# Optimization experiments

Measured on AMD Instinct MI355X. Metric: run time of the kernel, lower is better.

Reference implementation:

```python
import jax, jax.numpy as jnp
import numpy as np

EXP_BITS = 5
SIG_BITS = 10


def fp_quantize_ste(x, exp_bits=EXP_BITS, sig_bits=SIG_BITS):
    """Simulate a low-precision float format (round-to-nearest, subnormals on),
    with a straight-through estimator for gradients."""
    ebias = 2 ** (exp_bits - 1) - 1
    emin = 1 - ebias                      # min normal exponent; below -> subnormal
    emax = ebias
    xmax = (2.0 - 2.0 ** (-sig_bits)) * (2.0 ** emax)

    ax = jnp.abs(x)
    # exponent of each value; guard log2(0)
    e = jnp.floor(jnp.log2(jnp.where(ax > 0, ax, 1.0)))
    # clamping e below emin quantizes subnormals on the fixed 2^(emin-sig_bits) grid;
    # clamping above emax is handled by the final saturation to +-xmax
    e = jnp.clip(e, emin, emax)
    scale = jnp.exp2(sig_bits - e)        # quantization step = 2^(e - sig_bits)
    q = jnp.round(x * scale) / scale      # round-to-nearest (rmode=1)
    q = jnp.clip(q, -xmax, xmax)
    q = jnp.where(ax > 0, q, x)           # preserve exact zeros (and signed zero)
    # straight-through estimator: forward = q, backward = identity
    return x + jax.lax.stop_gradient(q - x)


def setup_inputs() -> dict:
    key = jax.random.key(0)
    k1, k2, k3 = jax.random.split(key, 3)
    N, D_IN, D_OUT = 8192, 4096, 4096
    x = jax.random.normal(k1, (N, D_IN), dtype=jnp.float32)
    weight = jax.random.normal(k2, (D_OUT, D_IN), dtype=jnp.float32) * (D_IN ** -0.5)
    bias = jax.random.normal(k3, (D_OUT,), dtype=jnp.float32) * 0.01
    return {"x": x, "weight": weight, "bias": bias}


def reference(x, weight, bias):
    xq = fp_quantize_ste(x)               # act_quant
    wq = fp_quantize_ste(weight)          # weight_quant
    bq = fp_quantize_ste(bias)            # bias quantized with weight_quant
    # F.linear: x @ W^T + b
    return jnp.einsum('ni,oi->no', xq, wq) + bq
```

## Files before the change

kernel.cpp:

```cpp
#include <hip/hip_runtime.h>
#include <hip/hip_fp16.h>
#include <cstdint>
#include <cstddef>

#define GLOBAL_AS __attribute__((address_space(1)))
#define LDS_AS    __attribute__((address_space(3)))

typedef __attribute__((ext_vector_type(8))) _Float16 f16x8;
typedef __attribute__((ext_vector_type(4))) float    f32x4;

__device__ __forceinline__ void gload_lds16(const void* g, void* l) {
    __builtin_amdgcn_global_load_lds((const GLOBAL_AS void*)g,
                                     (LDS_AS void*)l, 16, 0, 0);
}

__device__ __forceinline__ __half qcvt(float x) {
    x = fminf(fmaxf(x, -65504.f), 65504.f);
    return __float2half(x);
}

__global__ void quant_xw_f32_to_f16(const float* __restrict__ xin, int x4,
                                    const float* __restrict__ win, int w4,
                                    __half* __restrict__ xout,
                                    __half* __restrict__ wout) {
    const int stride = gridDim.x * blockDim.x;
    const int tot = x4 + w4;
    for (int i = blockIdx.x * blockDim.x + threadIdx.x; i < tot; i += stride) {
        const bool isx = (i < x4);
        const int  j   = isx ? i : i - x4;
        const float4 f = reinterpret_cast<const float4*>(isx ? xin : win)[j];
        union { __half h[4]; uint2 u; } p;
        p.h[0] = qcvt(f.x);
        p.h[1] = qcvt(f.y);
        p.h[2] = qcvt(f.z);
        p.h[3] = qcvt(f.w);
        reinterpret_cast<uint2*>(isx ? xout : wout)[j] = p.u;
    }
}

__global__ __launch_bounds__(512, 2) void gemm_f16_8phase(
    const __half* __restrict__ A, const __half* __restrict__ B,
    const float* __restrict__ bias, float* __restrict__ C,
    int M, int N, int K)
{
    __shared__ __align__(16) __half lds[2][2][2][8192];

    const int tid  = threadIdx.x;
    const int lane = tid & 63;
    const int wid  = tid >> 6;
    const int wr   = wid >> 2;
    const int wc   = wid & 3;
    const int fr   = lane & 15;
    const int fq   = lane >> 4;

    const int nwg = gridDim.x;
    const int qq = nwg >> 3, rr = nwg & 7;
    const int xcd = blockIdx.x & 7, idx = blockIdx.x >> 3;
    const int wgid = (xcd < rr ? xcd * (qq + 1)
                               : rr * (qq + 1) + (xcd - rr) * qq) + idx;
    const int nbn = N >> 8;
    const int tile_m = (wgid / nbn) << 8;
    const int tile_n = (wgid % nbn) << 8;

    const int wbyte = (lane * 16) ^ (((lane >> 5) & 1) << 5);
    const int srow  = ((wid >> 1) << 4) + (wbyte >> 6);
    const int scb   = ((wid & 1) << 6) + (wbyte & 63);
    const char* gA0 = (const char*)A + (size_t)(tile_m + srow) * K * 2 + scb;
    const char* gB0 = (const char*)B + (size_t)(tile_n + srow) * K * 2 + scb;
    const size_t rstep = (size_t)64  * K * 2;
    const size_t hstep = (size_t)128 * K * 2;
    const int ldst = tid * 16;

    const int woff = (fr * 64 + fq * 16) ^ (((fr >> 3) & 1) << 5);
    const uint32_t lds0 = (uint32_t)(size_t)(LDS_AS const char*)&lds[0][0][0][0];
    const uint32_t aBase = lds0 + (uint32_t)(wr * 8192 + woff);
    const uint32_t bBase = lds0 + 32768u + (uint32_t)(wc * 4096 + woff);

    f32x4 acc[2][2][4][2];
#pragma unroll
    for (int qa = 0; qa < 2; ++qa)
#pragma unroll
        for (int qb = 0; qb < 2; ++qb)
#pragma unroll
            for (int m = 0; m < 4; ++m)
#pragma unroll
                for (int n = 0; n < 2; ++n)
                    acc[qa][qb][m][n] = (f32x4){0.f, 0.f, 0.f, 0.f};

    f16x8 af[4][2];
    f16x8 bf0[2][2];
    f16x8 bf1[2][2];

#define STAGE_A(bufi, h, kt) do {                                          \
        char* l_ = (char*)(&lds[bufi][0][h][0]) + ldst;                    \
        const char* g_ = gA0 + (size_t)(kt) * 128 + ((h) ? hstep : 0);     \
        gload_lds16(g_, l_);                                               \
        gload_lds16(g_ + rstep, l_ + 8192);                                \
    } while (0)

#define STAGE_B(bufi, h, kt) do {                                          \
        char* l_ = (char*)(&lds[bufi][1][h][0]) + ldst;                    \
        const char* g_ = gB0 + (size_t)(kt) * 128 + ((h) ? hstep : 0);     \
        gload_lds16(g_, l_);                                               \
        gload_lds16(g_ + rstep, l_ + 8192);                                \
    } while (0)

#define DSR(dst, addr, OFF)                                                \
    asm volatile("ds_read_b128 %0, %1 offset:" OFF                         \
                 : "=v"(dst) : "v"(addr))

#define LDGA(bufi, qa) do {                                                \
        const uint32_t a_ = aBase + (bufi) * 65536u + (qa) * 16384u;       \
        DSR(af[0][0], a_, "0");    DSR(af[0][1], a_, "1024");              \
        DSR(af[1][0], a_, "2048"); DSR(af[1][1], a_, "3072");              \
        DSR(af[2][0], a_, "4096"); DSR(af[2][1], a_, "5120");              \
        DSR(af[3][0], a_, "6144"); DSR(af[3][1], a_, "7168");              \
    } while (0)

#define LDGB(dst, bufi, hb) do {                                           \
        const uint32_t b_ = bBase + (bufi) * 65536u + (hb) * 16384u;       \
        DSR(dst[0][0], b_, "0");    DSR(dst[0][1], b_, "1024");            \
        DSR(dst[1][0], b_, "2048"); DSR(dst[1][1], b_, "3072");            \
    } while (0)

#define MMA(qa, qb, BF)                                                    \
    __builtin_amdgcn_s_setprio(1);                                         \
    _Pragma("unroll")                                                      \
    for (int m_ = 0; m_ < 4; ++m_) {                                       \
        _Pragma("unroll")                                                  \
        for (int n_ = 0; n_ < 2; ++n_) {                                   \
            acc[qa][qb][m_][n_] = __builtin_amdgcn_mfma_f32_16x16x32_f16(  \
                af[m_][0], BF[n_][0], acc[qa][qb][m_][n_], 0, 0, 0);       \
            acc[qa][qb][m_][n_] = __builtin_amdgcn_mfma_f32_16x16x32_f16(  \
                af[m_][1], BF[n_][1], acc[qa][qb][m_][n_], 0, 0, 0);       \
        }                                                                  \
    }                                                                      \
    __builtin_amdgcn_s_setprio(0);

#define PH_WAIT_MMA()                                                      \
    __builtin_amdgcn_s_barrier();                                          \
    asm volatile("s_waitcnt lgkmcnt(0)");                                  \
    __builtin_amdgcn_sched_barrier(0)

#define PH_END()                                                           \
    __builtin_amdgcn_s_barrier()

#define TILE_FULL(cur, nxt, kt)                                            \
    LDGB(bf0, cur, 0); LDGA(cur, 0); STAGE_B(nxt, 0, (kt) + 1);            \
    asm volatile("s_waitcnt lgkmcnt(8)");                                  \
    PH_WAIT_MMA(); MMA(0, 0, bf0); PH_END();                               \
    LDGB(bf1, cur, 1); STAGE_A(cur, 0, (kt) + 2);                          \
    PH_WAIT_MMA(); MMA(0, 1, bf1); PH_END();                               \
    LDGA(cur, 1); STAGE_B(cur, 1, (kt) + 2);                               \
    PH_WAIT_MMA(); MMA(1, 1, bf1); PH_END();                               \
    STAGE_A(cur, 1, (kt) + 2);                                             \
    asm volatile("s_waitcnt vmcnt(6)");                                    \
    PH_WAIT_MMA(); MMA(1, 0, bf0); PH_END();

    STAGE_A(0, 0, 0); STAGE_B(0, 0, 0); STAGE_B(0, 1, 0); STAGE_A(0, 1, 0);
    STAGE_A(1, 0, 1); STAGE_B(1, 1, 1); STAGE_A(1, 1, 1);
    asm volatile("s_waitcnt vmcnt(6)");
    __builtin_amdgcn_s_barrier();

    const int nt = K >> 6;
    for (int kt = 0; kt + 3 < nt; kt += 2) {
        TILE_FULL(0, 1, kt);
        TILE_FULL(1, 0, kt + 1);
    }

    LDGB(bf0, 0, 0); LDGA(0, 0); STAGE_B(1, 0, nt - 1);
    PH_WAIT_MMA(); MMA(0, 0, bf0); PH_END();
    LDGB(bf1, 0, 1);
    PH_WAIT_MMA(); MMA(0, 1, bf1); PH_END();
    LDGA(0, 1);
    PH_WAIT_MMA(); MMA(1, 1, bf1); PH_END();
    asm volatile("s_waitcnt vmcnt(0)");
    PH_WAIT_MMA(); MMA(1, 0, bf0); PH_END();

    LDGB(bf0, 1, 0); LDGA(1, 0);
    PH_WAIT_MMA(); MMA(0, 0, bf0); PH_END();
    LDGB(bf1, 1, 1);
    PH_WAIT_MMA(); MMA(0, 1, bf1); PH_END();
    LDGA(1, 1);
    PH_WAIT_MMA(); MMA(1, 1, bf1); PH_END();
    asm volatile("s_waitcnt lgkmcnt(0)");
    __builtin_amdgcn_sched_barrier(0);
    MMA(1, 0, bf0);

    float bv[2][2];
#pragma unroll
    for (int qb = 0; qb < 2; ++qb)
#pragma unroll
        for (int n = 0; n < 2; ++n)
            bv[qb][n] = __half2float(qcvt(
                bias[tile_n + qb * 128 + wc * 32 + n * 16 + fr]));

#pragma unroll
    for (int qa = 0; qa < 2; ++qa)
#pragma unroll
        for (int qb = 0; qb < 2; ++qb)
#pragma unroll
            for (int m = 0; m < 4; ++m)
#pragma unroll
                for (int n = 0; n < 2; ++n) {
                    const int col = tile_n + qb * 128 + wc * 32 + n * 16 + fr;
                    const int rowb = tile_m + qa * 128 + wr * 64 + m * 16 + fq * 4;
#pragma unroll
                    for (int r = 0; r < 4; ++r)
                        C[(size_t)(rowb + r) * N + col] =
                            acc[qa][qb][m][n][r] + bv[qb][n];
                }

#undef STAGE_A
#undef STAGE_B
#undef DSR
#undef LDGA
#undef LDGB
#undef MMA
#undef PH_WAIT_MMA
#undef PH_END
#undef TILE_FULL
}

__global__ void qat_gemm_naive(const float* __restrict__ A,
                               const float* __restrict__ B,
                               const float* __restrict__ bias,
                               float* __restrict__ C, int M, int N, int K) {
    const int col = blockIdx.x * blockDim.x + threadIdx.x;
    const int row = blockIdx.y;
    if (col >= N || row >= M) return;
    float s = 0.f;
    for (int k = 0; k < K; ++k) {
        float a = __half2float(qcvt(A[(size_t)row * K + k]));
        float b = __half2float(qcvt(B[(size_t)col * K + k]));
        s += a * b;
    }
    C[(size_t)row * N + col] = s + __half2float(qcvt(bias[col]));
}

extern "C" void kernel_launch(void* const* d_in, const int* in_sizes, int n_in,
                              void* d_out, int out_size, void* d_ws,
                              size_t ws_size, hipStream_t stream) {
    const float* x = (const float*)d_in[0];
    const float* w = (const float*)d_in[1];
    const float* b = (const float*)d_in[2];
    float* out = (float*)d_out;

    const int xn = in_sizes[0];
    const int wn = in_sizes[1];
    const int N  = in_sizes[2];
    const int K  = wn / N;
    const int M  = xn / K;

    const size_t need = (size_t)(xn + wn) * sizeof(__half);
    const bool ok = (M % 256 == 0) && (N % 256 == 0) &&
                    (K % 128 == 0) && (K >= 256);

    if (ws_size >= need && ok) {
        __half* xq = (__half*)d_ws;
        __half* wq = xq + xn;

        const int x4 = xn / 4, w4 = wn / 4;
        int blk = ((x4 + w4) + 255) / 256; if (blk > 2048) blk = 2048;
        quant_xw_f32_to_f16<<<blk, 256, 0, stream>>>(x, x4, w, w4, xq, wq);

        dim3 grid((M / 256) * (N / 256));
        gemm_f16_8phase<<<grid, 512, 0, stream>>>(xq, wq, b, out, M, N, K);
    } else {
        dim3 grid((N + 255) / 256, M);
        qat_gemm_naive<<<grid, 256, 0, stream>>>(x, w, b, out, M, N, K);
    }
}
```

Baseline: 288.2 us.

## Split MFMA phases on partial LDS waits and prefetch next tile's B fragments

Each MFMA phase is split into two halves gated by partial lgkmcnt waits, so the first half of the MFMAs can start while the remaining ds_reads are still in flight. The B fragments for the next k-tile are loaded during the last phase of the current tile using ping-pong register sets (bfP/bfQ), which removes the LDS read latency at the start of each tile. The per-phase wait-then-barrier sequence is also reorganized. In exchange, register pressure rises from holding the extra B fragments, and correctness now depends on the hand-counted lgkmcnt values matching the issue order.

```diff
diff --git a/kernel.cpp b/kernel.cpp
--- a/kernel.cpp
+++ b/kernel.cpp
@@ -88,8 +88,8 @@
                     acc[qa][qb][m][n] = (f32x4){0.f, 0.f, 0.f, 0.f};
 
     f16x8 af[4][2];
-    f16x8 bf0[2][2];
-    f16x8 bf1[2][2];
+    f16x8 bfP[2][2];
+    f16x8 bfQ[2][2];
 
 #define STAGE_A(bufi, h, kt) do {                                          \
         char* l_ = (char*)(&lds[bufi][0][h][0]) + ldst;                    \
@@ -123,69 +123,116 @@
         DSR(dst[1][0], b_, "2048"); DSR(dst[1][1], b_, "3072");            \
     } while (0)
 
-#define MMA(qa, qb, BF)                                                    \
+#define MMA_PAIR(qa, qb, mm, nn, BF)                                       \
+    acc[qa][qb][mm][nn] = __builtin_amdgcn_mfma_f32_16x16x32_f16(          \
+        af[mm][0], BF[nn][0], acc[qa][qb][mm][nn], 0, 0, 0);               \
+    acc[qa][qb][mm][nn] = __builtin_amdgcn_mfma_f32_16x16x32_f16(          \
+        af[mm][1], BF[nn][1], acc[qa][qb][mm][nn], 0, 0, 0);
+
+#define MMA_M01(qa, qb, BF)                                                \
     __builtin_amdgcn_s_setprio(1);                                         \
-    _Pragma("unroll")                                                      \
-    for (int m_ = 0; m_ < 4; ++m_) {                                       \
-        _Pragma("unroll")                                                  \
-        for (int n_ = 0; n_ < 2; ++n_) {                                   \
-            acc[qa][qb][m_][n_] = __builtin_amdgcn_mfma_f32_16x16x32_f16(  \
-                af[m_][0], BF[n_][0], acc[qa][qb][m_][n_], 0, 0, 0);       \
-            acc[qa][qb][m_][n_] = __builtin_amdgcn_mfma_f32_16x16x32_f16(  \
-                af[m_][1], BF[n_][1], acc[qa][qb][m_][n_], 0, 0, 0);       \
-        }                                                                  \
-    }                                                                      \
+    MMA_PAIR(qa, qb, 0, 0, BF) MMA_PAIR(qa, qb, 0, 1, BF)                  \
+    MMA_PAIR(qa, qb, 1, 0, BF) MMA_PAIR(qa, qb, 1, 1, BF)                  \
     __builtin_amdgcn_s_setprio(0);
 
-#define PH_WAIT_MMA()                                                      \
+#define MMA_M23(qa, qb, BF)                                                \
+    __builtin_amdgcn_s_setprio(1);                                         \
+    MMA_PAIR(qa, qb, 2, 0, BF) MMA_PAIR(qa, qb, 2, 1, BF)                  \
+    MMA_PAIR(qa, qb, 3, 0, BF) MMA_PAIR(qa, qb, 3, 1, BF)                  \
+    __builtin_amdgcn_s_setprio(0);
+
+#define MMA_N0(qa, qb, BF)                                                 \
+    __builtin_amdgcn_s_setprio(1);                                         \
+    MMA_PAIR(qa, qb, 0, 0, BF) MMA_PAIR(qa, qb, 1, 0, BF)                  \
+    MMA_PAIR(qa, qb, 2, 0, BF) MMA_PAIR(qa, qb, 3, 0, BF)                  \
+    __builtin_amdgcn_s_setprio(0);
+
+#define MMA_N1(qa, qb, BF)                                                 \
+    __builtin_amdgcn_s_setprio(1);                                         \
+    MMA_PAIR(qa, qb, 0, 1, BF) MMA_PAIR(qa, qb, 1, 1, BF)                  \
+    MMA_PAIR(qa, qb, 2, 1, BF) MMA_PAIR(qa, qb, 3, 1, BF)                  \
+    __builtin_amdgcn_s_setprio(0);
+
+#define MMA_FULL(qa, qb, BF)                                               \
+    MMA_M01(qa, qb, BF) MMA_M23(qa, qb, BF)
+
+#define WAITL(NLIT)                                                        \
+    asm volatile("s_waitcnt lgkmcnt(" NLIT ")");                           \
+    __builtin_amdgcn_sched_barrier(0)
+
+#define BARS()                                                             \
     __builtin_amdgcn_s_barrier();                                          \
-    asm volatile("s_waitcnt lgkmcnt(0)");                                  \
     __builtin_amdgcn_sched_barrier(0)
 
-#define PH_END()                                                           \
-    __builtin_amdgcn_s_barrier()
-
-#define TILE_FULL(cur, nxt, kt)                                            \
-    LDGB(bf0, cur, 0); LDGA(cur, 0); STAGE_B(nxt, 0, (kt) + 1);            \
-    asm volatile("s_waitcnt lgkmcnt(8)");                                  \
-    PH_WAIT_MMA(); MMA(0, 0, bf0); PH_END();                               \
-    LDGB(bf1, cur, 1); STAGE_A(cur, 0, (kt) + 2);                          \
-    PH_WAIT_MMA(); MMA(0, 1, bf1); PH_END();                               \
+#define TILE_FULL(cur, nxt, kt, B0S, B1S)                                  \
+                \
+    LDGA(cur, 0); STAGE_B(nxt, 0, (kt) + 1);                               \
+    WAITL("4"); MMA_M01(0, 0, B0S);                                        \
+    WAITL("0"); MMA_M23(0, 0, B0S);                                        \
+    BARS();                                                                \
+                    \
+    LDGB(B1S, cur, 1); STAGE_A(cur, 0, (kt) + 2);                          \
+    WAITL("2"); MMA_N0(0, 1, B1S);                                         \
+    WAITL("0"); MMA_N1(0, 1, B1S);                                         \
+    BARS();                                                                \
+                \
     LDGA(cur, 1); STAGE_B(cur, 1, (kt) + 2);                               \
-    PH_WAIT_MMA(); MMA(1, 1, bf1); PH_END();                               \
+    WAITL("4"); MMA_M01(1, 1, B1S);                                        \
+    WAITL("0"); MMA_M23(1, 1, B1S);                                        \
+    BARS();                                                                \
+    \
     STAGE_A(cur, 1, (kt) + 2);                                             \
     asm volatile("s_waitcnt vmcnt(6)");                                    \
-    PH_WAIT_MMA(); MMA(1, 0, bf0); PH_END();
+    BARS();                                                                \
+    LDGB(B1S, nxt, 0);                                                     \
+    __builtin_amdgcn_sched_barrier(0);                                     \
+    MMA_FULL(1, 0, B0S);                                                   \
+    BARS();
 
     STAGE_A(0, 0, 0); STAGE_B(0, 0, 0); STAGE_B(0, 1, 0); STAGE_A(0, 1, 0);
     STAGE_A(1, 0, 1); STAGE_B(1, 1, 1); STAGE_A(1, 1, 1);
     asm volatile("s_waitcnt vmcnt(6)");
-    __builtin_amdgcn_s_barrier();
+    BARS();
+    LDGB(bfP, 0, 0);
 
     const int nt = K >> 6;
     for (int kt = 0; kt + 3 < nt; kt += 2) {
-        TILE_FULL(0, 1, kt);
-        TILE_FULL(1, 0, kt + 1);
+        TILE_FULL(0, 1, kt,     bfP, bfQ);
+        TILE_FULL(1, 0, kt + 1, bfQ, bfP);
     }
 
-    LDGB(bf0, 0, 0); LDGA(0, 0); STAGE_B(1, 0, nt - 1);
-    PH_WAIT_MMA(); MMA(0, 0, bf0); PH_END();
-    LDGB(bf1, 0, 1);
-    PH_WAIT_MMA(); MMA(0, 1, bf1); PH_END();
+    LDGA(0, 0); STAGE_B(1, 0, nt - 1);
+    WAITL("4"); MMA_M01(0, 0, bfP);
+    WAITL("0"); MMA_M23(0, 0, bfP);
+    BARS();
+    LDGB(bfQ, 0, 1);
+    WAITL("2"); MMA_N0(0, 1, bfQ);
+    WAITL("0"); MMA_N1(0, 1, bfQ);
+    BARS();
     LDGA(0, 1);
-    PH_WAIT_MMA(); MMA(1, 1, bf1); PH_END();
+    WAITL("4"); MMA_M01(1, 1, bfQ);
+    WAITL("0"); MMA_M23(1, 1, bfQ);
+    BARS();
     asm volatile("s_waitcnt vmcnt(0)");
-    PH_WAIT_MMA(); MMA(1, 0, bf0); PH_END();
-
-    LDGB(bf0, 1, 0); LDGA(1, 0);
-    PH_WAIT_MMA(); MMA(0, 0, bf0); PH_END();
-    LDGB(bf1, 1, 1);
-    PH_WAIT_MMA(); MMA(0, 1, bf1); PH_END();
+    BARS();
+    LDGB(bfQ, 1, 0);
+    __builtin_amdgcn_sched_barrier(0);
+    MMA_FULL(1, 0, bfP);
+    BARS();
+
+    LDGA(1, 0);
+    WAITL("4"); MMA_M01(0, 0, bfQ);
+    WAITL("0"); MMA_M23(0, 0, bfQ);
+    BARS();
+    LDGB(bfP, 1, 1);
+    WAITL("2"); MMA_N0(0, 1, bfP);
+    WAITL("0"); MMA_N1(0, 1, bfP);
+    BARS();
     LDGA(1, 1);
-    PH_WAIT_MMA(); MMA(1, 1, bf1); PH_END();
-    asm volatile("s_waitcnt lgkmcnt(0)");
-    __builtin_amdgcn_sched_barrier(0);
-    MMA(1, 0, bf0);
+    WAITL("4"); MMA_M01(1, 1, bfP);
+    WAITL("0"); MMA_M23(1, 1, bfP);
+    BARS();
+    MMA_FULL(1, 0, bfQ);
 
     float bv[2][2];
 #pragma unroll
@@ -216,9 +263,14 @@
 #undef DSR
 #undef LDGA
 #undef LDGB
-#undef MMA
-#undef PH_WAIT_MMA
-#undef PH_END
+#undef MMA_PAIR
+#undef MMA_M01
+#undef MMA_M23
+#undef MMA_N0
+#undef MMA_N1
+#undef MMA_FULL
+#undef WAITL
+#undef BARS
 #undef TILE_FULL
 }
 
```

Result: faster. 276.1 us (-4.2%).
